# Kernel tuning notes

Hardware: AMD Instinct MI355X
Metric: run time of the kernel (lower is better)

The kernel has to match this reference:

```python
import jax, jax.numpy as jnp
import numpy as np

NUM_CLASSES = 1000
FEAT_DIM = 512
BATCH = 16384


def setup_inputs() -> dict:
    key = jax.random.key(0)
    k1, k2, k3 = jax.random.split(key, 3)
    x = jax.random.normal(k1, (BATCH, FEAT_DIM), dtype=jnp.float32)
    labels = jax.random.randint(k2, (BATCH,), 0, NUM_CLASSES, dtype=jnp.int64)
    centers = jax.random.normal(k3, (NUM_CLASSES, FEAT_DIM), dtype=jnp.float32)
    margin = jnp.ones((1,), dtype=jnp.float32)
    return {"x": x, "labels": labels, "centers": centers, "margin": margin}


def reference(x, labels, centers, margin):
    # squared euclidean distances: [B, C]
    distmat = (
        jnp.sum(x * x, axis=1, keepdims=True)
        + jnp.sum(centers * centers, axis=1)[None, :]
        - 2.0 * (x @ centers.T)
    )
    B, C = distmat.shape
    onehot = labels[:, None] == jnp.arange(C, dtype=labels.dtype)[None, :]  # [B, C]
    # distance to the true-class center
    dist = jnp.sum(jnp.where(onehot, distmat, 0.0), axis=1)  # [B]
    # min distance over all other classes (mask true class with +inf)
    dist_min = jnp.min(jnp.where(onehot, jnp.inf, distmat), axis=1)  # [B]
    m = margin[0]
    loss = jnp.sum(jnp.maximum(m + dist - dist_min, 0.0)) / B
    return loss
```

## Files before the change

kernel.cpp:

```cpp
#include <hip/hip_runtime.h>
#include <hip/hip_bf16.h>

#define BATCH 16384
#define NCLS  1000
#define NPAD  1024
#define FDIM  512

#define CBLK_STRIDE 270336
#define TAIL_OFF    262144

typedef __bf16 bf16x4 __attribute__((ext_vector_type(4)));
typedef __bf16 bf16x8 __attribute__((ext_vector_type(8)));
typedef float  f32x16 __attribute__((ext_vector_type(16)));

#define GLOBAL_AS __attribute__((address_space(1)))
#define LDS_AS    __attribute__((address_space(3)))

#define VMCNT(n) asm volatile("s_waitcnt vmcnt(" #n ")" ::: "memory")
#define LGKM0()  asm volatile("s_waitcnt lgkmcnt(0)" ::: "memory")
#define BAR()    do { LGKM0(); __builtin_amdgcn_s_barrier(); \
                      __builtin_amdgcn_sched_barrier(0); } while (0)

__global__ __launch_bounds__(64) void prep_centers(
    const float* __restrict__ centers, char* __restrict__ cbt)
{
    const int c = blockIdx.x, t = threadIdx.x;
    const int cblk = c >> 8, cl = c & 255;
    char* base = cbt + (size_t)cblk * CBLK_STRIDE;

    float4 f0 = make_float4(0.f, 0.f, 0.f, 0.f);
    float4 f1 = make_float4(0.f, 0.f, 0.f, 0.f);
    if (c < NCLS) {
        f0 = *(const float4*)(centers + (size_t)c * FDIM + t * 8);
        f1 = *(const float4*)(centers + (size_t)c * FDIM + t * 8 + 4);
    }
    bf16x8 b;
    b[0] = (__bf16)f0.x; b[1] = (__bf16)f0.y; b[2] = (__bf16)f0.z; b[3] = (__bf16)f0.w;
    b[4] = (__bf16)f1.x; b[5] = (__bf16)f1.y; b[6] = (__bf16)f1.z; b[7] = (__bf16)f1.w;
    *(bf16x8*)(base + (t >> 2) * 16384 + (t & 3) * 4096 + cl * 16) = b;

    float ssum = f0.x*f0.x + f0.y*f0.y + f0.z*f0.z + f0.w*f0.w
               + f1.x*f1.x + f1.y*f1.y + f1.z*f1.z + f1.w*f1.w;
    #pragma unroll
    for (int o = 32; o > 0; o >>= 1) ssum += __shfl_down(ssum, o);
    if (t == 0) {
        const float hf = (c < NCLS) ? (-0.5f * ssum) : -1e30f;
        const __bf16 h = (__bf16)hf;
        const __bf16 l = (c < NCLS) ? (__bf16)(hf - (float)h) : (__bf16)0.f;
        bf16x8 tl;
        #pragma unroll
        for (int e = 0; e < 8; ++e) tl[e] = (__bf16)0.f;
        tl[0] = h; tl[1] = l;
        *(bf16x8*)(base + TAIL_OFF + cl * 16) = tl;
        bf16x8 z;
        #pragma unroll
        for (int e = 0; e < 8; ++e) z[e] = (__bf16)0.f;
        *(bf16x8*)(base + TAIL_OFF + 4096 + cl * 16) = z;
    }
}

struct B4 { float4 a, b, c, d; };

__global__ __launch_bounds__(512, 2) void trip_main(
    const float* __restrict__ x, const int* __restrict__ labels,
    const char* __restrict__ cbt, float* __restrict__ mxp,
    float* __restrict__ dap)
{
    extern __shared__ char lds[];
    const int t    = threadIdx.x;
    const int lane = t & 63;
    const int w    = t >> 6;
    const int wN   = w & 3, wM = w >> 2;
    const int l31  = lane & 31, hi = lane >> 5;
    const int bid  = blockIdx.x;
    const int cblk = bid >> 6;
    const int bblk = bid & 63;
    const int class0 = cblk * 256;
    const int row0   = bblk * 256;
    const char* cbB  = cbt + (size_t)cblk * CBLK_STRIDE;

    auto stageA = [&](int ko, int ai) {
        const char* src = cbB + ko * 16384 + w * 1024 + lane * 16;
        char* dst = lds + ai * 16384 + w * 1024 + lane * 16;
        __builtin_amdgcn_global_load_lds((const GLOBAL_AS void*)src,
                                         (LDS_AS void*)dst, 16, 0, 0);
        __builtin_amdgcn_global_load_lds((const GLOBAL_AS void*)(src + 8192),
                                         (LDS_AS void*)(dst + 8192), 16, 0, 0);
    };
    auto loadB = [&](int ko, B4& br) {
        const float* src = x + (size_t)row0 * FDIM + ko * 32
                         + (size_t)(w * 32 + (lane >> 3)) * FDIM + (lane & 7) * 4;
        br.a = *(const float4*)(src);
        br.b = *(const float4*)(src +  8 * FDIM);
        br.c = *(const float4*)(src + 16 * FDIM);
        br.d = *(const float4*)(src + 24 * FDIM);
    };
    auto cv4 = [](float4 f) {
        bf16x4 v;
        v[0] = (__bf16)f.x; v[1] = (__bf16)f.y;
        v[2] = (__bf16)f.z; v[3] = (__bf16)f.w;
        return v;
    };
    auto writeB = [&](const B4& br, int bi) {
        char* dst = lds + 49152 + bi * 16384 + ((lane & 7) >> 1) * 4096
                  + (w * 32 + (lane >> 3)) * 16 + (lane & 1) * 8;
        *(bf16x4*)(dst          ) = cv4(br.a);
        *(bf16x4*)(dst + 128    ) = cv4(br.b);
        *(bf16x4*)(dst + 256    ) = cv4(br.c);
        *(bf16x4*)(dst + 384    ) = cv4(br.d);
    };

    f32x16 acc[4][2];
    #pragma unroll
    for (int mi = 0; mi < 4; ++mi)
        #pragma unroll
        for (int ni = 0; ni < 2; ++ni)
            #pragma unroll
            for (int r = 0; r < 16; ++r) acc[mi][ni][r] = 0.f;

    auto compute = [&](int buf) {
        const char* A = lds + buf * 16384;
        const char* B = lds + 49152 + buf * 16384;
        #pragma unroll
        for (int ks = 0; ks < 2; ++ks) {
            const int chunk = ks * 2 + hi;
            bf16x8 a[4], b[2];
            #pragma unroll
            for (int mi = 0; mi < 4; ++mi)
                a[mi] = *(const bf16x8*)(A + chunk * 4096 + (wM * 128 + mi * 32 + l31) * 16);
            #pragma unroll
            for (int ni = 0; ni < 2; ++ni)
                b[ni] = *(const bf16x8*)(B + chunk * 4096 + (wN * 64 + ni * 32 + l31) * 16);
            #pragma unroll
            for (int mi = 0; mi < 4; ++mi)
                #pragma unroll
                for (int ni = 0; ni < 2; ++ni)
                    acc[mi][ni] = __builtin_amdgcn_mfma_f32_32x32x16_bf16(
                        a[mi], b[ni], acc[mi][ni], 0, 0, 0);
        }
    };

    const int lab0 = labels[row0 + wN * 64 + l31];
    const int lab1 = labels[row0 + wN * 64 + 32 + l31];
    {
        const char* src = cbB + TAIL_OFF + t * 16;
        char* dst = lds + 98304 + t * 16;
        __builtin_amdgcn_global_load_lds((const GLOBAL_AS void*)src,
                                         (LDS_AS void*)dst, 16, 0, 0);
    }
    B4 brA, brB;
    stageA(0, 0); loadB(0, brA);
    __builtin_amdgcn_sched_barrier(0);
    stageA(1, 1); loadB(1, brB);
    VMCNT(6);
    writeB(brA, 0);
    BAR();

    #pragma unroll
    for (int tt = 0; tt < 16; ++tt) {
        const int cur = tt % 3, wr = (tt + 1) % 3, pre = (tt + 2) % 3;
        if (tt < 14) {
            stageA(tt + 2, pre);
            if (tt & 1) loadB(tt + 2, brB);
            else        loadB(tt + 2, brA);
            VMCNT(6);
        } else {
            VMCNT(0);
        }
        if (tt < 15) {
            if (tt & 1) writeB(brA, wr);
            else        writeB(brB, wr);
        }
        compute(cur);
        BAR();
    }

    {
        const char* T = lds + 98304;
        bf16x8 bt;
        #pragma unroll
        for (int e = 0; e < 8; ++e) bt[e] = (__bf16)0.f;
        if (hi == 0) { bt[0] = (__bf16)1.0f; bt[1] = (__bf16)1.0f; }
        #pragma unroll
        for (int mi = 0; mi < 4; ++mi) {
            bf16x8 a = *(const bf16x8*)(T + hi * 4096 + (wM * 128 + mi * 32 + l31) * 16);
            #pragma unroll
            for (int ni = 0; ni < 2; ++ni)
                acc[mi][ni] = __builtin_amdgcn_mfma_f32_32x32x16_bf16(
                    a, bt, acc[mi][ni], 0, 0, 0);
        }
    }

    const int labBase = class0 + wM * 128 + hi * 4;
    const int labA0 = lab0 - labBase;
    const int labA1 = lab1 - labBase;
    float MX0 = -3e38f, MX1 = -3e38f, DA0 = -3e38f, DA1 = -3e38f;
    #pragma unroll
    for (int mi = 0; mi < 4; ++mi) {
        #pragma unroll
        for (int r = 0; r < 16; ++r) {
            const int pat = mi * 32 + (r & 3) + 8 * (r >> 2);
            {
                const float a = acc[mi][0][r];
                const bool is = (labA0 == pat);
                MX0 = fmaxf(MX0, is ? -3e38f : a);
                DA0 = is ? a : DA0;
            }
            {
                const float a = acc[mi][1][r];
                const bool is = (labA1 == pat);
                MX1 = fmaxf(MX1, is ? -3e38f : a);
                DA1 = is ? a : DA1;
            }
        }
    }
    MX0 = fmaxf(MX0, __shfl_xor(MX0, 32));
    DA0 = fmaxf(DA0, __shfl_xor(DA0, 32));
    MX1 = fmaxf(MX1, __shfl_xor(MX1, 32));
    DA1 = fmaxf(DA1, __shfl_xor(DA1, 32));

    float* sc = (float*)(lds + 104 * 1024);
    const int i0 = (wN * 2 + 0) * 32 + l31;
    const int i1 = (wN * 2 + 1) * 32 + l31;
    if (wM == 1 && hi == 0) {
        sc[i0] = MX0; sc[256 + i0] = DA0;
        sc[i1] = MX1; sc[256 + i1] = DA1;
    }
    __syncthreads();
    if (wM == 0 && hi == 0) {
        const float M0 = fmaxf(MX0, sc[i0]),  D0 = fmaxf(DA0, sc[256 + i0]);
        const float M1 = fmaxf(MX1, sc[i1]),  D1 = fmaxf(DA1, sc[256 + i1]);
        const int rg = row0 + wN * 64 + l31;
        mxp[cblk * BATCH + rg]      = M0;
        dap[cblk * BATCH + rg]      = D0;
        mxp[cblk * BATCH + rg + 32] = M1;
        dap[cblk * BATCH + rg + 32] = D1;
    }
}

__global__ __launch_bounds__(256) void combine1(
    const float* __restrict__ mxp, const float* __restrict__ dap,
    const float* __restrict__ margin, float* __restrict__ partial)
{
    const int t = threadIdx.x;
    const int row = blockIdx.x * 256 + t;
    float mx = mxp[row];
    mx = fmaxf(mx, mxp[BATCH + row]);
    mx = fmaxf(mx, mxp[2 * BATCH + row]);
    mx = fmaxf(mx, mxp[3 * BATCH + row]);
    float da = dap[row];
    da = fmaxf(da, dap[BATCH + row]);
    da = fmaxf(da, dap[2 * BATCH + row]);
    da = fmaxf(da, dap[3 * BATCH + row]);
    float loss = fmaxf(margin[0] - 2.f * da + 2.f * mx, 0.f);
    __shared__ float red[4];
    #pragma unroll
    for (int o = 32; o > 0; o >>= 1) loss += __shfl_down(loss, o);
    if ((t & 63) == 0) red[t >> 6] = loss;
    __syncthreads();
    if (t == 0) partial[blockIdx.x] = red[0] + red[1] + red[2] + red[3];
}

__global__ __launch_bounds__(64) void combine2(
    const float* __restrict__ partial, float* __restrict__ out)
{
    float s = partial[threadIdx.x];
    #pragma unroll
    for (int o = 32; o > 0; o >>= 1) s += __shfl_down(s, o);
    if (threadIdx.x == 0) out[0] = s * (1.0f / BATCH);
}

extern "C" void kernel_launch(void* const* d_in, const int* in_sizes, int n_in,
                              void* d_out, int out_size, void* d_ws, size_t ws_size,
                              hipStream_t stream)
{
    const float* x       = (const float*)d_in[0];
    const int*   labels  = (const int*)d_in[1];
    const float* centers = (const float*)d_in[2];
    const float* margin  = (const float*)d_in[3];
    float* out = (float*)d_out;

    char* ws = (char*)d_ws;
    char*  cbt  = ws;
    float* mxp  = (float*)(ws + 1081344);
    float* dap  = (float*)(ws + 1343488);
    float* part = (float*)(ws + 1605632);

    (void)hipFuncSetAttribute((const void*)trip_main,
                              hipFuncAttributeMaxDynamicSharedMemorySize, 110592);

    prep_centers<<<NPAD, 64, 0, stream>>>(centers, cbt);
    trip_main<<<256, 512, 110592, stream>>>(x, labels, cbt, mxp, dap);
    combine1<<<64, 256, 0, stream>>>(mxp, dap, margin, part);
    combine2<<<1, 64, 0, stream>>>(part, out);
}
```

Measured before the change: 33.50 us.

## Double K-tile depth in main GEMM pipeline and fuse final reduction via atomics

The main kernel's K step grows from 32 to 64 and the pipeline moves from triple to double buffering. Each step now stages twice as much data and runs twice as many MFMAs, halving the loop iterations and barriers. LDS use rises to about 132KB, so launch bounds drop to one block per CU, which costs occupancy. The two combine kernels become one that uses atomicAdd into an output zeroed in prep_centers, removing a launch; the tail block shrinks to 4KB.

```diff
diff --git a/kernel.cpp b/kernel.cpp
--- a/kernel.cpp
+++ b/kernel.cpp
@@ -6,7 +6,7 @@
 #define NPAD  1024
 #define FDIM  512
 
-#define CBLK_STRIDE 270336
+#define CBLK_STRIDE 266240
 #define TAIL_OFF    262144
 
 typedef __bf16 bf16x4 __attribute__((ext_vector_type(4)));
@@ -22,11 +22,13 @@
                       __builtin_amdgcn_sched_barrier(0); } while (0)
 
 __global__ __launch_bounds__(64) void prep_centers(
-    const float* __restrict__ centers, char* __restrict__ cbt)
+    const float* __restrict__ centers, char* __restrict__ cbt,
+    float* __restrict__ out)
 {
     const int c = blockIdx.x, t = threadIdx.x;
     const int cblk = c >> 8, cl = c & 255;
     char* base = cbt + (size_t)cblk * CBLK_STRIDE;
+    if (c == 0 && t == 0) out[0] = 0.f;
 
     float4 f0 = make_float4(0.f, 0.f, 0.f, 0.f);
     float4 f1 = make_float4(0.f, 0.f, 0.f, 0.f);
@@ -37,7 +39,7 @@
     bf16x8 b;
     b[0] = (__bf16)f0.x; b[1] = (__bf16)f0.y; b[2] = (__bf16)f0.z; b[3] = (__bf16)f0.w;
     b[4] = (__bf16)f1.x; b[5] = (__bf16)f1.y; b[6] = (__bf16)f1.z; b[7] = (__bf16)f1.w;
-    *(bf16x8*)(base + (t >> 2) * 16384 + (t & 3) * 4096 + cl * 16) = b;
+    *(bf16x8*)(base + (t >> 3) * 32768 + (t & 7) * 4096 + cl * 16) = b;
 
     float ssum = f0.x*f0.x + f0.y*f0.y + f0.z*f0.z + f0.w*f0.w
                + f1.x*f1.x + f1.y*f1.y + f1.z*f1.z + f1.w*f1.w;
@@ -52,16 +54,12 @@
         for (int e = 0; e < 8; ++e) tl[e] = (__bf16)0.f;
         tl[0] = h; tl[1] = l;
         *(bf16x8*)(base + TAIL_OFF + cl * 16) = tl;
-        bf16x8 z;
-        #pragma unroll
-        for (int e = 0; e < 8; ++e) z[e] = (__bf16)0.f;
-        *(bf16x8*)(base + TAIL_OFF + 4096 + cl * 16) = z;
-    }
-}
-
-struct B4 { float4 a, b, c, d; };
-
-__global__ __launch_bounds__(512, 2) void trip_main(
+    }
+}
+
+struct B8 { float4 a, b, c, d, e, f, g, h; };
+
+__global__ __launch_bounds__(512, 1) void trip_main(
     const float* __restrict__ x, const int* __restrict__ labels,
     const char* __restrict__ cbt, float* __restrict__ mxp,
     float* __restrict__ dap)
@@ -80,20 +78,25 @@
     const char* cbB  = cbt + (size_t)cblk * CBLK_STRIDE;
 
     auto stageA = [&](int ko, int ai) {
-        const char* src = cbB + ko * 16384 + w * 1024 + lane * 16;
-        char* dst = lds + ai * 16384 + w * 1024 + lane * 16;
-        __builtin_amdgcn_global_load_lds((const GLOBAL_AS void*)src,
-                                         (LDS_AS void*)dst, 16, 0, 0);
-        __builtin_amdgcn_global_load_lds((const GLOBAL_AS void*)(src + 8192),
-                                         (LDS_AS void*)(dst + 8192), 16, 0, 0);
-    };
-    auto loadB = [&](int ko, B4& br) {
-        const float* src = x + (size_t)row0 * FDIM + ko * 32
-                         + (size_t)(w * 32 + (lane >> 3)) * FDIM + (lane & 7) * 4;
+        const char* src = cbB + ko * 32768 + t * 16;
+        char* dst = lds + ai * 32768 + t * 16;
+        #pragma unroll
+        for (int j = 0; j < 4; ++j)
+            __builtin_amdgcn_global_load_lds(
+                (const GLOBAL_AS void*)(src + j * 8192),
+                (LDS_AS void*)(dst + j * 8192), 16, 0, 0);
+    };
+    auto loadB = [&](int ko, B8& br) {
+        const float* src = x + (size_t)(row0 + w * 32 + (lane >> 3)) * FDIM
+                         + ko * 64 + (lane & 7) * 4;
         br.a = *(const float4*)(src);
-        br.b = *(const float4*)(src +  8 * FDIM);
-        br.c = *(const float4*)(src + 16 * FDIM);
-        br.d = *(const float4*)(src + 24 * FDIM);
+        br.b = *(const float4*)(src + 32);
+        br.c = *(const float4*)(src +  8 * FDIM);
+        br.d = *(const float4*)(src +  8 * FDIM + 32);
+        br.e = *(const float4*)(src + 16 * FDIM);
+        br.f = *(const float4*)(src + 16 * FDIM + 32);
+        br.g = *(const float4*)(src + 24 * FDIM);
+        br.h = *(const float4*)(src + 24 * FDIM + 32);
     };
     auto cv4 = [](float4 f) {
         bf16x4 v;
@@ -101,13 +104,17 @@
         v[2] = (__bf16)f.z; v[3] = (__bf16)f.w;
         return v;
     };
-    auto writeB = [&](const B4& br, int bi) {
-        char* dst = lds + 49152 + bi * 16384 + ((lane & 7) >> 1) * 4096
+    auto writeB = [&](const B8& br, int bi) {
+        char* dst = lds + 65536 + bi * 32768 + ((lane & 7) >> 1) * 4096
                   + (w * 32 + (lane >> 3)) * 16 + (lane & 1) * 8;
-        *(bf16x4*)(dst          ) = cv4(br.a);
-        *(bf16x4*)(dst + 128    ) = cv4(br.b);
-        *(bf16x4*)(dst + 256    ) = cv4(br.c);
-        *(bf16x4*)(dst + 384    ) = cv4(br.d);
+        *(bf16x4*)(dst              ) = cv4(br.a);
+        *(bf16x4*)(dst + 4 * 4096   ) = cv4(br.b);
+        *(bf16x4*)(dst + 128        ) = cv4(br.c);
+        *(bf16x4*)(dst + 4 * 4096 + 128) = cv4(br.d);
+        *(bf16x4*)(dst + 256        ) = cv4(br.e);
+        *(bf16x4*)(dst + 4 * 4096 + 256) = cv4(br.f);
+        *(bf16x4*)(dst + 384        ) = cv4(br.g);
+        *(bf16x4*)(dst + 4 * 4096 + 384) = cv4(br.h);
     };
 
     f32x16 acc[4][2];
@@ -119,10 +126,10 @@
             for (int r = 0; r < 16; ++r) acc[mi][ni][r] = 0.f;
 
     auto compute = [&](int buf) {
-        const char* A = lds + buf * 16384;
-        const char* B = lds + 49152 + buf * 16384;
-        #pragma unroll
-        for (int ks = 0; ks < 2; ++ks) {
+        const char* A = lds + buf * 32768;
+        const char* B = lds + 65536 + buf * 32768;
+        #pragma unroll
+        for (int ks = 0; ks < 4; ++ks) {
             const int chunk = ks * 2 + hi;
             bf16x8 a[4], b[2];
             #pragma unroll
@@ -142,48 +149,47 @@
 
     const int lab0 = labels[row0 + wN * 64 + l31];
     const int lab1 = labels[row0 + wN * 64 + 32 + l31];
-    {
+    if (t < 256) {
         const char* src = cbB + TAIL_OFF + t * 16;
-        char* dst = lds + 98304 + t * 16;
+        char* dst = lds + 131072 + t * 16;
         __builtin_amdgcn_global_load_lds((const GLOBAL_AS void*)src,
                                          (LDS_AS void*)dst, 16, 0, 0);
     }
-    B4 brA, brB;
+    B8 brA, brB;
     stageA(0, 0); loadB(0, brA);
     __builtin_amdgcn_sched_barrier(0);
-    stageA(1, 1); loadB(1, brB);
-    VMCNT(6);
+    loadB(1, brB); stageA(1, 1);
+    VMCNT(12);
     writeB(brA, 0);
     BAR();
 
     #pragma unroll
-    for (int tt = 0; tt < 16; ++tt) {
-        const int cur = tt % 3, wr = (tt + 1) % 3, pre = (tt + 2) % 3;
-        if (tt < 14) {
-            stageA(tt + 2, pre);
+    for (int tt = 0; tt < 8; ++tt) {
+        if (tt >= 1 && tt <= 6) stageA(tt + 1, (tt + 1) & 1);
+        if (tt <= 5) {
             if (tt & 1) loadB(tt + 2, brB);
             else        loadB(tt + 2, brA);
-            VMCNT(6);
-        } else {
-            VMCNT(0);
-        }
-        if (tt < 15) {
-            if (tt & 1) writeB(brA, wr);
-            else        writeB(brB, wr);
-        }
-        compute(cur);
+        }
+        if (tt <= 5)      VMCNT(12);
+        else if (tt == 6) VMCNT(4);
+        else              VMCNT(0);
+        if (tt <= 6) {
+            if (tt & 1) writeB(brA, (tt + 1) & 1);
+            else        writeB(brB, (tt + 1) & 1);
+        }
+        compute(tt & 1);
         BAR();
     }
 
     {
-        const char* T = lds + 98304;
+        const char* T = lds + 131072;
         bf16x8 bt;
         #pragma unroll
         for (int e = 0; e < 8; ++e) bt[e] = (__bf16)0.f;
         if (hi == 0) { bt[0] = (__bf16)1.0f; bt[1] = (__bf16)1.0f; }
         #pragma unroll
         for (int mi = 0; mi < 4; ++mi) {
-            bf16x8 a = *(const bf16x8*)(T + hi * 4096 + (wM * 128 + mi * 32 + l31) * 16);
+            bf16x8 a = *(const bf16x8*)(T + (wM * 128 + mi * 32 + l31) * 16);
             #pragma unroll
             for (int ni = 0; ni < 2; ++ni)
                 acc[mi][ni] = __builtin_amdgcn_mfma_f32_32x32x16_bf16(
@@ -219,7 +225,7 @@
     MX1 = fmaxf(MX1, __shfl_xor(MX1, 32));
     DA1 = fmaxf(DA1, __shfl_xor(DA1, 32));
 
-    float* sc = (float*)(lds + 104 * 1024);
+    float* sc = (float*)(lds + 65536);
     const int i0 = (wN * 2 + 0) * 32 + l31;
     const int i1 = (wN * 2 + 1) * 32 + l31;
     if (wM == 1 && hi == 0) {
@@ -238,36 +244,24 @@
     }
 }
 
-__global__ __launch_bounds__(256) void combine1(
+__global__ __launch_bounds__(256) void combine(
     const float* __restrict__ mxp, const float* __restrict__ dap,
-    const float* __restrict__ margin, float* __restrict__ partial)
+    const float* __restrict__ margin, float* __restrict__ out)
 {
     const int t = threadIdx.x;
     const int row = blockIdx.x * 256 + t;
-    float mx = mxp[row];
-    mx = fmaxf(mx, mxp[BATCH + row]);
-    mx = fmaxf(mx, mxp[2 * BATCH + row]);
-    mx = fmaxf(mx, mxp[3 * BATCH + row]);
-    float da = dap[row];
-    da = fmaxf(da, dap[BATCH + row]);
-    da = fmaxf(da, dap[2 * BATCH + row]);
-    da = fmaxf(da, dap[3 * BATCH + row]);
+    float mx = fmaxf(fmaxf(mxp[row], mxp[BATCH + row]),
+                     fmaxf(mxp[2 * BATCH + row], mxp[3 * BATCH + row]));
+    float da = fmaxf(fmaxf(dap[row], dap[BATCH + row]),
+                     fmaxf(dap[2 * BATCH + row], dap[3 * BATCH + row]));
     float loss = fmaxf(margin[0] - 2.f * da + 2.f * mx, 0.f);
     __shared__ float red[4];
     #pragma unroll
     for (int o = 32; o > 0; o >>= 1) loss += __shfl_down(loss, o);
     if ((t & 63) == 0) red[t >> 6] = loss;
     __syncthreads();
-    if (t == 0) partial[blockIdx.x] = red[0] + red[1] + red[2] + red[3];
-}
-
-__global__ __launch_bounds__(64) void combine2(
-    const float* __restrict__ partial, float* __restrict__ out)
-{
-    float s = partial[threadIdx.x];
-    #pragma unroll
-    for (int o = 32; o > 0; o >>= 1) s += __shfl_down(s, o);
-    if (threadIdx.x == 0) out[0] = s * (1.0f / BATCH);
+    if (t == 0)
+        atomicAdd(out, (red[0] + red[1] + red[2] + red[3]) * (1.0f / BATCH));
 }
 
 extern "C" void kernel_launch(void* const* d_in, const int* in_sizes, int n_in,
@@ -282,15 +276,13 @@
 
     char* ws = (char*)d_ws;
     char*  cbt  = ws;
-    float* mxp  = (float*)(ws + 1081344);
-    float* dap  = (float*)(ws + 1343488);
-    float* part = (float*)(ws + 1605632);
+    float* mxp  = (float*)(ws + 1064960);
+    float* dap  = (float*)(ws + 1327104);
 
     (void)hipFuncSetAttribute((const void*)trip_main,
-                              hipFuncAttributeMaxDynamicSharedMemorySize, 110592);
-
-    prep_centers<<<NPAD, 64, 0, stream>>>(centers, cbt);
-    trip_main<<<256, 512, 110592, stream>>>(x, labels, cbt, mxp, dap);
-    combine1<<<64, 256, 0, stream>>>(mxp, dap, margin, part);
-    combine2<<<1, 64, 0, stream>>>(part, out);
-}
+                              hipFuncAttributeMaxDynamicSharedMemorySize, 135168);
+
+    prep_centers<<<NPAD, 64, 0, stream>>>(centers, cbt, out);
+    trip_main<<<256, 512, 135168, stream>>>(x, labels, cbt, mxp, dap);
+    combine<<<64, 256, 0, stream>>>(mxp, dap, margin, out);
+}
```

After: 33.95 us. About the same (+1.3%).
